# Performance work log

Hardware: AMD Instinct MI355X
Metric: run time of the kernel (lower is better)

The kernel has to match this reference:

```python
import jax, jax.numpy as jnp
import numpy as np

NHEAD = 8  # matches init_kwargs

M_NODES = 20000
D_MODEL = 512
N_EDGES = 640000


def setup_inputs() -> dict:
    key = jax.random.key(0)
    ks = jax.random.split(key, 8)
    sc = 1.0 / np.sqrt(D_MODEL)
    return {
        "s": jax.random.normal(ks[0], (M_NODES, D_MODEL), dtype=jnp.float32),
        "edge_index": jax.random.randint(ks[1], (2, N_EDGES), 0, M_NODES, dtype=jnp.int64),
        "Wq": jax.random.normal(ks[2], (D_MODEL, D_MODEL), dtype=jnp.float32) * sc,
        "bq": jax.random.normal(ks[3], (D_MODEL,), dtype=jnp.float32) * sc,
        "Wkv": jax.random.normal(ks[4], (2 * D_MODEL, D_MODEL), dtype=jnp.float32) * sc,
        "bkv": jax.random.normal(ks[5], (2 * D_MODEL,), dtype=jnp.float32) * sc,
        "Wo": jax.random.normal(ks[6], (D_MODEL, D_MODEL), dtype=jnp.float32) * sc,
        "bo": jax.random.normal(ks[7], (D_MODEL,), dtype=jnp.float32) * sc,
    }


def reference(s, edge_index, Wq, bq, Wkv, bkv, Wo, bo):
    M, C = s.shape
    H = NHEAD
    Dh = C // H
    scale = 1.0 / np.sqrt(Dh).astype(np.float32)

    q = (s @ Wq.T + bq).reshape(M, H, Dh)            # [M,H,Dh]
    kv = (s @ Wkv.T + bkv).reshape(M, H, 2 * Dh)     # [M,H,2Dh]
    k, v = kv[..., :Dh], kv[..., Dh:]

    src, tgt = edge_index[0], edge_index[1]

    # per-edge attention logits [E,H]
    a = jnp.einsum('ehc,ehc->eh', q[tgt], k[src]) * scale

    # segment softmax over edges sharing the same target node
    a_max = jax.ops.segment_max(a, tgt, num_segments=M)        # [M,H]
    ex = jnp.exp(a - a_max[tgt])                               # [E,H]
    denom = jax.ops.segment_sum(ex, tgt, num_segments=M)      # [M,H]
    attn = ex / denom[tgt]                                     # [E,H]

    # weighted message aggregation: scatter-sum over target nodes
    o_msg = attn[..., None] * v[src]                           # [E,H,Dh]
    o = jax.ops.segment_sum(o_msg, tgt, num_segments=M)       # [M,H,Dh]
    o = o.reshape(M, C)
    return o @ Wo.T + bo
```

## Files before the change

kernel.cpp:

```cpp
#include <hip/hip_runtime.h>
#include <cmath>

#define MN 20000
#define DM 512
#define NE 640000
#define CAP 128

typedef short  bf16x8 __attribute__((ext_vector_type(8)));
typedef float  f32x4  __attribute__((ext_vector_type(4)));
typedef ushort u16x4  __attribute__((ext_vector_type(4)));

__device__ __forceinline__ ushort f2b(float x) {
    unsigned u = __builtin_bit_cast(unsigned, x);
    u += 0x7FFF + ((u >> 16) & 1);
    return (ushort)(u >> 16);
}
__device__ __forceinline__ float b2f(ushort b) {
    return __builtin_bit_cast(float, (unsigned)b << 16);
}

#define NS4   (MN * DM / 4)
#define NWC4  (1536 * 512 / 4)
#define NWO4  (512 * 512 / 4)
#define NB4   (1536 / 4)

__device__ __forceinline__ const float* wc_src_row(int r, const float* Wq, const float* Wkv) {
    if (r < 512) return Wq + ((size_t)r << 9);
    if (r < 1024) { int h = (r - 512) >> 6, j = (r - 512) & 63;  return Wkv + ((size_t)(h * 128 + j) << 9); }
    { int h = (r - 1024) >> 6, j = (r - 1024) & 63; return Wkv + ((size_t)(h * 128 + 64 + j) << 9); }
}

__global__ void conv_all_k(const float* __restrict__ s, const float* __restrict__ Wq,
                           const float* __restrict__ Wkv, const float* __restrict__ Wo,
                           const float* __restrict__ bq, const float* __restrict__ bkv,
                           const int* __restrict__ tgt, int* __restrict__ counts,
                           ushort* __restrict__ s_b, ushort* __restrict__ Wc_b,
                           ushort* __restrict__ Wo_b, float* __restrict__ bc)
{
    int i = blockIdx.x * blockDim.x + threadIdx.x;
    if (i < NE) atomicAdd(&counts[tgt[i]], 1);
    if (i < NS4) {
        float4 v = ((const float4*)s)[i];
        ushort4 o = { f2b(v.x), f2b(v.y), f2b(v.z), f2b(v.w) };
        ((ushort4*)s_b)[i] = o;
        return;
    }
    i -= NS4;
    if (i < NWC4) {
        int e = i * 4, row = e >> 9, col = e & 511;
        float4 v = *(const float4*)(wc_src_row(row, Wq, Wkv) + col);
        ushort4 o = { f2b(v.x), f2b(v.y), f2b(v.z), f2b(v.w) };
        ((ushort4*)Wc_b)[i] = o;
        return;
    }
    i -= NWC4;
    if (i < NWO4) {
        float4 v = ((const float4*)Wo)[i];
        ushort4 o = { f2b(v.x), f2b(v.y), f2b(v.z), f2b(v.w) };
        ((ushort4*)Wo_b)[i] = o;
        return;
    }
    i -= NWO4;
    if (i < NB4) {
#pragma unroll
        for (int u = 0; u < 4; ++u) {
            int r = i * 4 + u;
            float v;
            if (r < 512) v = bq[r];
            else if (r < 1024) { int h = (r - 512) >> 6, j = (r - 512) & 63;  v = bkv[h * 128 + j]; }
            else               { int h = (r - 1024) >> 6, j = (r - 1024) & 63; v = bkv[h * 128 + 64 + j]; }
            bc[r] = v;
        }
    }
}

template<int SPLIT, bool OUTBF>
__global__ __launch_bounds__(256) void gemm_mfma(
    const ushort* __restrict__ Ah, const ushort* __restrict__ Al,
    const ushort* __restrict__ Bh, const ushort* __restrict__ Bl,
    const float* __restrict__ bias, void* __restrict__ Cout, int M, int N, int K)
{
    __shared__ ushort lds[4 * 4096];
    const int tid = threadIdx.x;
    const int row0 = blockIdx.x * 128, col0 = blockIdx.y * 128;
    const int wid = tid >> 6, l = tid & 63;
    const int wm = (wid >> 1) * 64, wn = (wid & 1) * 64;
    const int fr = l & 15, g = l >> 4;
    const int fcb = g << 4;

    f32x4 acc[4][4] = {};

    for (int k0 = 0; k0 < K; k0 += 32) {
        __syncthreads();
#pragma unroll
        for (int c = 0; c < 2; ++c) {
            const int lb  = c * 4096 + tid * 16;
            const int r   = lb >> 6;
            const int cbs = (lb & 63) ^ ((r & 6) << 3);
            const int ar  = min(row0 + r, M - 1);
            const int br  = col0 + r;
            const size_t aoff = (size_t)ar * K + k0 + (cbs >> 1);
            const size_t boff = (size_t)br * K + k0 + (cbs >> 1);
            __builtin_amdgcn_global_load_lds(
                (const __attribute__((address_space(1))) void*)(Ah + aoff),
                (__attribute__((address_space(3))) void*)&lds[0 * 4096 + (lb >> 1)], 16, 0, 0);
            __builtin_amdgcn_global_load_lds(
                (const __attribute__((address_space(1))) void*)(Bh + boff),
                (__attribute__((address_space(3))) void*)&lds[1 * 4096 + (lb >> 1)], 16, 0, 0);
            if (SPLIT == 3) {
                __builtin_amdgcn_global_load_lds(
                    (const __attribute__((address_space(1))) void*)(Al + aoff),
                    (__attribute__((address_space(3))) void*)&lds[2 * 4096 + (lb >> 1)], 16, 0, 0);
                __builtin_amdgcn_global_load_lds(
                    (const __attribute__((address_space(1))) void*)(Bl + boff),
                    (__attribute__((address_space(3))) void*)&lds[3 * 4096 + (lb >> 1)], 16, 0, 0);
            }
        }
        __syncthreads();

        bf16x8 ah[4], bh[4], al[4], bl[4];
#pragma unroll
        for (int m = 0; m < 4; ++m) {
            const int r  = wm + m * 16 + fr;
            const int cb = fcb ^ ((r & 6) << 3);
            ah[m] = *(const bf16x8*)&lds[0 * 4096 + r * 32 + (cb >> 1)];
            if (SPLIT == 3) al[m] = *(const bf16x8*)&lds[2 * 4096 + r * 32 + (cb >> 1)];
        }
#pragma unroll
        for (int n = 0; n < 4; ++n) {
            const int r  = wn + n * 16 + fr;
            const int cb = fcb ^ ((r & 6) << 3);
            bh[n] = *(const bf16x8*)&lds[1 * 4096 + r * 32 + (cb >> 1)];
            if (SPLIT == 3) bl[n] = *(const bf16x8*)&lds[3 * 4096 + r * 32 + (cb >> 1)];
        }
#pragma unroll
        for (int m = 0; m < 4; ++m)
#pragma unroll
            for (int n = 0; n < 4; ++n) {
                acc[m][n] = __builtin_amdgcn_mfma_f32_16x16x32_bf16(ah[m], bh[n], acc[m][n], 0, 0, 0);
                if (SPLIT == 3) {
                    acc[m][n] = __builtin_amdgcn_mfma_f32_16x16x32_bf16(ah[m], bl[n], acc[m][n], 0, 0, 0);
                    acc[m][n] = __builtin_amdgcn_mfma_f32_16x16x32_bf16(al[m], bh[n], acc[m][n], 0, 0, 0);
                }
            }
    }

#pragma unroll
    for (int n = 0; n < 4; ++n) {
        const int cg = col0 + wn + n * 16 + fr;
        const float bv = bias[cg];
#pragma unroll
        for (int m = 0; m < 4; ++m) {
#pragma unroll
            for (int j = 0; j < 4; ++j) {
                const int rg = row0 + wm + m * 16 + g * 4 + j;
                if (rg < M) {
                    const float v = acc[m][n][j] + bv;
                    if (OUTBF) ((ushort*)Cout)[(size_t)rg * N + cg] = f2b(v);
                    else       ((float*)Cout)[(size_t)rg * N + cg] = v;
                }
            }
        }
    }
}

__global__ __launch_bounds__(1024) void scan_counts_k(
    const int* __restrict__ counts, int* __restrict__ indptr,
    int* __restrict__ dbase, int M)
{
    __shared__ int part[1024];
    __shared__ int hist[128];
    const int t  = threadIdx.x;
    if (t < 128) hist[t] = 0;
    __syncthreads();
    const int CH = (M + 1023) / 1024;
    const int base = t * CH;
    int sum = 0;
    for (int i = 0; i < CH; ++i) {
        int idx = base + i;
        if (idx < M) {
            int c = counts[idx];
            sum += c;
            atomicAdd(&hist[127 - min(c, 127)], 1);
        }
    }
    part[t] = sum;
    __syncthreads();
    for (int off = 1; off < 1024; off <<= 1) {
        int v = (t >= off) ? part[t - off] : 0;
        __syncthreads();
        part[t] += v;
        __syncthreads();
    }
    int excl = part[t] - sum;
    for (int i = 0; i < CH; ++i) {
        int idx = base + i;
        if (idx < M) { indptr[idx] = excl; excl += counts[idx]; }
    }
    if (t == 1023) indptr[M] = part[1023];
    __syncthreads();
    if (t == 0) {
        int run = 0;
        for (int b = 0; b < 128; ++b) { int v = hist[b]; dbase[b] = run; run += v; }
    }
}

__global__ void scatter_fused_k(const int* __restrict__ src, const int* __restrict__ tgt,
                                const int* __restrict__ indptr, int* __restrict__ cursor,
                                int* __restrict__ slot_off, const int* __restrict__ counts,
                                const int* __restrict__ dbase, int* __restrict__ dcur,
                                int* __restrict__ perm, int E, int M)
{
    int e = blockIdx.x * blockDim.x + threadIdx.x;
    if (e < E) {
        int t   = tgt[e];
        int pos = atomicAdd(&cursor[t], 1);
        slot_off[indptr[t] + pos] = src[e] * 3072;
    }
    if (e < M) {
        int b = 127 - min(counts[e], 127);
        int pos = atomicAdd(&dcur[b], 1);
        perm[dbase[b] + pos] = e;
    }
}

__global__ __launch_bounds__(256, 4) void attn9_k(
    const ushort* __restrict__ qkv, const int* __restrict__ indptr,
    const int* __restrict__ slot_off, const int* __restrict__ perm,
    ushort* __restrict__ obh)
{
    __shared__ int slots[4][CAP];
    const int w = threadIdx.x >> 6;
    const int l = threadIdx.x & 63;
    const int node = perm[blockIdx.x * 4 + w];
    const int beg = indptr[node], end = indptr[node + 1];
    const int d = end - beg;
    const int dc = min(d, CAP);

    for (int i = l; i < dc; i += 64) slots[w][i] = slot_off[beg + i];
    __syncthreads();

    const char* base = (const char*)qkv + (l << 4);

    float qf[8];
    {
        bf16x8 qv = *(const bf16x8*)(base + (size_t)node * 3072);
#pragma unroll
        for (int j = 0; j < 8; ++j) qf[j] = b2f((ushort)qv[j]);
    }

    float acc[8] = {};
    float ssum = 0.f;

    int i = 0;
    for (; i + 8 <= dc; i += 8) {
        const int4 sa = *(const int4*)&slots[w][i];
        const int4 sb = *(const int4*)&slots[w][i + 4];
        const char* bp[8] = { base + sa.x, base + sa.y, base + sa.z, base + sa.w,
                              base + sb.x, base + sb.y, base + sb.z, base + sb.w };
        bf16x8 kk[8], vv[8];
#pragma unroll
        for (int u = 0; u < 8; ++u) {
            kk[u] = __builtin_nontemporal_load((const bf16x8*)(bp[u] + 1024));
            vv[u] = __builtin_nontemporal_load((const bf16x8*)(bp[u] + 2048));
        }
        float p[8];
#pragma unroll
        for (int u = 0; u < 8; ++u) {
            float pu = 0.f;
#pragma unroll
            for (int j = 0; j < 8; ++j) pu = fmaf(qf[j], b2f((ushort)kk[u][j]), pu);
            p[u] = pu;
        }
#pragma unroll
        for (int u = 0; u < 8; ++u) p[u] += __shfl_xor(p[u], 1);
#pragma unroll
        for (int u = 0; u < 8; ++u) p[u] += __shfl_xor(p[u], 2);
#pragma unroll
        for (int u = 0; u < 8; ++u) p[u] += __shfl_xor(p[u], 4);
        float wt[8];
#pragma unroll
        for (int u = 0; u < 8; ++u) { wt[u] = __expf(p[u] * 0.125f); ssum += wt[u]; }
#pragma unroll
        for (int u = 0; u < 8; ++u)
#pragma unroll
            for (int j = 0; j < 8; ++j) acc[j] = fmaf(wt[u], b2f((ushort)vv[u][j]), acc[j]);
    }
    for (; i < d; ++i) {
        const int so = (i < CAP) ? slots[w][i] : slot_off[beg + i];
        const char* b0 = base + so;
        bf16x8 k0 = __builtin_nontemporal_load((const bf16x8*)(b0 + 1024));
        bf16x8 v0 = __builtin_nontemporal_load((const bf16x8*)(b0 + 2048));
        float p0 = 0.f;
#pragma unroll
        for (int j = 0; j < 8; ++j) p0 = fmaf(qf[j], b2f((ushort)k0[j]), p0);
        p0 += __shfl_xor(p0, 1); p0 += __shfl_xor(p0, 2); p0 += __shfl_xor(p0, 4);
        const float w0 = __expf(p0 * 0.125f);
        ssum += w0;
#pragma unroll
        for (int j = 0; j < 8; ++j) acc[j] = fmaf(w0, b2f((ushort)v0[j]), acc[j]);
    }

    const float inv = (d > 0) ? 1.f / ssum : 0.f;
    u16x4 ph0, ph1;
    ph0[0] = f2b(acc[0] * inv); ph0[1] = f2b(acc[1] * inv);
    ph0[2] = f2b(acc[2] * inv); ph0[3] = f2b(acc[3] * inv);
    ph1[0] = f2b(acc[4] * inv); ph1[1] = f2b(acc[5] * inv);
    ph1[2] = f2b(acc[6] * inv); ph1[3] = f2b(acc[7] * inv);
    const size_t ob_off = (size_t)node * 512 + (l << 3);
    __builtin_nontemporal_store(ph0, (u16x4*)(obh + ob_off));
    __builtin_nontemporal_store(ph1, (u16x4*)(obh + ob_off + 4));
}

extern "C" void kernel_launch(void* const* d_in, const int* in_sizes, int n_in,
                              void* d_out, int out_size, void* d_ws, size_t ws_size,
                              hipStream_t stream)
{
    const float* s   = (const float*)d_in[0];
    const int*   eix = (const int*)d_in[1];
    const float* Wq  = (const float*)d_in[2];
    const float* bq  = (const float*)d_in[3];
    const float* Wkv = (const float*)d_in[4];
    const float* bkv = (const float*)d_in[5];
    const float* Wo  = (const float*)d_in[6];
    const float* bo  = (const float*)d_in[7];
    float* out = (float*)d_out;

    char* ws = (char*)d_ws;
    auto take = [&](size_t bytes) { char* p = ws; ws += (bytes + 255) & ~(size_t)255; return p; };
    ushort* qkv_b  = (ushort*)take((size_t)MN * 1536 * 2);
    ushort* s_b    = (ushort*)take((size_t)MN * 512 * 2);
    ushort* obh    = (ushort*)take((size_t)MN * 512 * 2);
    ushort* Wc_b   = (ushort*)take((size_t)1536 * 512 * 2);
    ushort* Wo_b   = (ushort*)take((size_t)512 * 512 * 2);
    float*  bc     = (float*)take(1536 * 4);
    int* counts    = (int*)take(MN * 4);
    int* cursor    = (int*)take(MN * 4);
    int* slot_off  = (int*)take((size_t)NE * 4);
    int* indptr    = (int*)take((MN + 4) * 4);
    int* dbase     = (int*)take(128 * 4);
    int* dcur      = (int*)take(128 * 4);
    int* perm      = (int*)take(MN * 4);

    hipMemsetAsync(counts, 0, MN * 4, stream);
    hipMemsetAsync(cursor, 0, MN * 4, stream);
    hipMemsetAsync(dcur, 0, 128 * 4, stream);

    const int convN = NS4 + NWC4 + NWO4 + NB4;
    conv_all_k<<<(convN + 255) / 256, 256, 0, stream>>>(s, Wq, Wkv, Wo, bq, bkv,
                                                        eix + NE, counts,
                                                        s_b, Wc_b, Wo_b, bc);

    scan_counts_k<<<1, 1024, 0, stream>>>(counts, indptr, dbase, MN);
    scatter_fused_k<<<NE / 256, 256, 0, stream>>>(eix, eix + NE, indptr, cursor,
                                                  slot_off, counts, dbase, dcur, perm, NE, MN);

    dim3 g1((MN + 127) / 128, 1536 / 128);
    gemm_mfma<1, true><<<g1, 256, 0, stream>>>(s_b, s_b, Wc_b, Wc_b, bc, qkv_b, MN, 1536, DM);

    attn9_k<<<MN / 4, 256, 0, stream>>>(qkv_b, indptr, slot_off, perm, obh);

    dim3 g2((MN + 127) / 128, 512 / 128);
    gemm_mfma<1, false><<<g2, 256, 0, stream>>>(obh, obh, Wo_b, Wo_b, bo, out, MN, 512, DM);
}
```

Baseline: 462.7 us.

## Bucket each node's edges by source-node tile for gather locality

Edges in each target's CSR segment are now grouped by source-node tile (src>>10, 20 tiles). This uses a second per-(target,tile) histogram, a per-node offset kernel and a tile-keyed scatter. Because concurrently running waves then tend to touch nearby source rows, the random K/V gathers should hit L2/MALL more often. Nontemporal loads and stores in the attention kernel become ordinary cached accesses so that this reuse can happen. The cost is an extra 1.6MB histogram with its memset, a second set of atomics, and one more small kernel launch.

```diff
diff --git a/kernel.cpp b/kernel.cpp
--- a/kernel.cpp
+++ b/kernel.cpp
@@ -5,10 +5,11 @@
 #define DM 512
 #define NE 640000
 #define CAP 128
+#define NT 20
+#define TSHIFT 10
 
 typedef short  bf16x8 __attribute__((ext_vector_type(8)));
 typedef float  f32x4  __attribute__((ext_vector_type(4)));
-typedef ushort u16x4  __attribute__((ext_vector_type(4)));
 
 __device__ __forceinline__ ushort f2b(float x) {
     unsigned u = __builtin_bit_cast(unsigned, x);
@@ -33,12 +34,17 @@
 __global__ void conv_all_k(const float* __restrict__ s, const float* __restrict__ Wq,
                            const float* __restrict__ Wkv, const float* __restrict__ Wo,
                            const float* __restrict__ bq, const float* __restrict__ bkv,
-                           const int* __restrict__ tgt, int* __restrict__ counts,
+                           const int* __restrict__ esrc, const int* __restrict__ etgt,
+                           int* __restrict__ counts, int* __restrict__ counts2,
                            ushort* __restrict__ s_b, ushort* __restrict__ Wc_b,
                            ushort* __restrict__ Wo_b, float* __restrict__ bc)
 {
     int i = blockIdx.x * blockDim.x + threadIdx.x;
-    if (i < NE) atomicAdd(&counts[tgt[i]], 1);
+    if (i < NE) {
+        int t = etgt[i];
+        atomicAdd(&counts[t], 1);
+        atomicAdd(&counts2[t * NT + (esrc[i] >> TSHIFT)], 1);
+    }
     if (i < NS4) {
         float4 v = ((const float4*)s)[i];
         ushort4 o = { f2b(v.x), f2b(v.y), f2b(v.z), f2b(v.w) };
@@ -205,17 +211,29 @@
     }
 }
 
+__global__ void tileoff_k(const int* __restrict__ indptr, const int* __restrict__ counts2,
+                          int* __restrict__ cursor2, int M)
+{
+    int n = blockIdx.x * blockDim.x + threadIdx.x;
+    if (n >= M) return;
+    int run = indptr[n];
+#pragma unroll
+    for (int j = 0; j < NT; ++j) {
+        cursor2[n * NT + j] = run;
+        run += counts2[n * NT + j];
+    }
+}
+
 __global__ void scatter_fused_k(const int* __restrict__ src, const int* __restrict__ tgt,
-                                const int* __restrict__ indptr, int* __restrict__ cursor,
-                                int* __restrict__ slot_off, const int* __restrict__ counts,
-                                const int* __restrict__ dbase, int* __restrict__ dcur,
-                                int* __restrict__ perm, int E, int M)
+                                int* __restrict__ cursor2, int* __restrict__ slot_off,
+                                const int* __restrict__ counts, const int* __restrict__ dbase,
+                                int* __restrict__ dcur, int* __restrict__ perm, int E, int M)
 {
     int e = blockIdx.x * blockDim.x + threadIdx.x;
     if (e < E) {
-        int t   = tgt[e];
-        int pos = atomicAdd(&cursor[t], 1);
-        slot_off[indptr[t] + pos] = src[e] * 3072;
+        int t = tgt[e], s = src[e];
+        int pos = atomicAdd(&cursor2[t * NT + (s >> TSHIFT)], 1);
+        slot_off[pos] = s * 3072;
     }
     if (e < M) {
         int b = 127 - min(counts[e], 127);
@@ -224,7 +242,7 @@
     }
 }
 
-__global__ __launch_bounds__(256, 4) void attn9_k(
+__global__ __launch_bounds__(256, 4) void attn11_k(
     const ushort* __restrict__ qkv, const int* __restrict__ indptr,
     const int* __restrict__ slot_off, const int* __restrict__ perm,
     ushort* __restrict__ obh)
@@ -261,8 +279,8 @@
         bf16x8 kk[8], vv[8];
 #pragma unroll
         for (int u = 0; u < 8; ++u) {
-            kk[u] = __builtin_nontemporal_load((const bf16x8*)(bp[u] + 1024));
-            vv[u] = __builtin_nontemporal_load((const bf16x8*)(bp[u] + 2048));
+            kk[u] = *(const bf16x8*)(bp[u] + 1024);
+            vv[u] = *(const bf16x8*)(bp[u] + 2048);
         }
         float p[8];
 #pragma unroll
@@ -289,8 +307,8 @@
     for (; i < d; ++i) {
         const int so = (i < CAP) ? slots[w][i] : slot_off[beg + i];
         const char* b0 = base + so;
-        bf16x8 k0 = __builtin_nontemporal_load((const bf16x8*)(b0 + 1024));
-        bf16x8 v0 = __builtin_nontemporal_load((const bf16x8*)(b0 + 2048));
+        bf16x8 k0 = *(const bf16x8*)(b0 + 1024);
+        bf16x8 v0 = *(const bf16x8*)(b0 + 2048);
         float p0 = 0.f;
 #pragma unroll
         for (int j = 0; j < 8; ++j) p0 = fmaf(qf[j], b2f((ushort)k0[j]), p0);
@@ -302,14 +320,14 @@
     }
 
     const float inv = (d > 0) ? 1.f / ssum : 0.f;
-    u16x4 ph0, ph1;
-    ph0[0] = f2b(acc[0] * inv); ph0[1] = f2b(acc[1] * inv);
-    ph0[2] = f2b(acc[2] * inv); ph0[3] = f2b(acc[3] * inv);
-    ph1[0] = f2b(acc[4] * inv); ph1[1] = f2b(acc[5] * inv);
-    ph1[2] = f2b(acc[6] * inv); ph1[3] = f2b(acc[7] * inv);
+    ushort4 ph0, ph1;
+    ph0.x = f2b(acc[0] * inv); ph0.y = f2b(acc[1] * inv);
+    ph0.z = f2b(acc[2] * inv); ph0.w = f2b(acc[3] * inv);
+    ph1.x = f2b(acc[4] * inv); ph1.y = f2b(acc[5] * inv);
+    ph1.z = f2b(acc[6] * inv); ph1.w = f2b(acc[7] * inv);
     const size_t ob_off = (size_t)node * 512 + (l << 3);
-    __builtin_nontemporal_store(ph0, (u16x4*)(obh + ob_off));
-    __builtin_nontemporal_store(ph1, (u16x4*)(obh + ob_off + 4));
+    *(ushort4*)(obh + ob_off)     = ph0;
+    *(ushort4*)(obh + ob_off + 4) = ph1;
 }
 
 extern "C" void kernel_launch(void* const* d_in, const int* in_sizes, int n_in,
@@ -335,7 +353,8 @@
     ushort* Wo_b   = (ushort*)take((size_t)512 * 512 * 2);
     float*  bc     = (float*)take(1536 * 4);
     int* counts    = (int*)take(MN * 4);
-    int* cursor    = (int*)take(MN * 4);
+    int* counts2   = (int*)take((size_t)MN * NT * 4);
+    int* cursor2   = (int*)take((size_t)MN * NT * 4);
     int* slot_off  = (int*)take((size_t)NE * 4);
     int* indptr    = (int*)take((MN + 4) * 4);
     int* dbase     = (int*)take(128 * 4);
@@ -343,22 +362,23 @@
     int* perm      = (int*)take(MN * 4);
 
     hipMemsetAsync(counts, 0, MN * 4, stream);
-    hipMemsetAsync(cursor, 0, MN * 4, stream);
+    hipMemsetAsync(counts2, 0, (size_t)MN * NT * 4, stream);
     hipMemsetAsync(dcur, 0, 128 * 4, stream);
 
     const int convN = NS4 + NWC4 + NWO4 + NB4;
     conv_all_k<<<(convN + 255) / 256, 256, 0, stream>>>(s, Wq, Wkv, Wo, bq, bkv,
-                                                        eix + NE, counts,
+                                                        eix, eix + NE, counts, counts2,
                                                         s_b, Wc_b, Wo_b, bc);
 
     scan_counts_k<<<1, 1024, 0, stream>>>(counts, indptr, dbase, MN);
-    scatter_fused_k<<<NE / 256, 256, 0, stream>>>(eix, eix + NE, indptr, cursor,
-                                                  slot_off, counts, dbase, dcur, perm, NE, MN);
+    tileoff_k<<<(MN + 255) / 256, 256, 0, stream>>>(indptr, counts2, cursor2, MN);
+    scatter_fused_k<<<NE / 256, 256, 0, stream>>>(eix, eix + NE, cursor2, slot_off,
+                                                  counts, dbase, dcur, perm, NE, MN);
 
     dim3 g1((MN + 127) / 128, 1536 / 128);
     gemm_mfma<1, true><<<g1, 256, 0, stream>>>(s_b, s_b, Wc_b, Wc_b, bc, qkv_b, MN, 1536, DM);
 
-    attn9_k<<<MN / 4, 256, 0, stream>>>(qkv_b, indptr, slot_off, perm, obh);
+    attn11_k<<<MN / 4, 256, 0, stream>>>(qkv_b, indptr, slot_off, perm, obh);
 
     dim3 g2((MN + 127) / 128, 512 / 128);
     gemm_mfma<1, false><<<g2, 256, 0, stream>>>(obh, obh, Wo_b, Wo_b, bo, out, MN, 512, DM);
```

After: 416.1 us. 10.1% less time.
